# Kernel tuning notes

Hardware: AMD Instinct MI355X
Metric: run time of the kernel (lower is better)

Reference implementation:

```python
import jax, jax.numpy as jnp
import numpy as np

B, N, E = 128, 256, 2048
BINS = 16

def _gcn(x, src, dst, W, b):
    # GCNConv with self-loops and symmetric deg^-1/2 normalization (PyG default).
    h = x @ W  # [N, Fout]
    deg = jnp.zeros(x.shape[0], x.dtype).at[dst].add(1.0) + 1.0  # +1 self-loop
    dinv = jax.lax.rsqrt(deg)
    coef = dinv[src] * dinv[dst]  # [E]
    agg = jnp.zeros_like(h).at[dst].add(h[src] * coef[:, None])
    return agg + h / deg[:, None] + b  # self-loop norm = 1/deg

def _gnn(x, ei, W1, b1, W2, b2, W3, b3):
    # x: [B,N,Fin], ei: [B,2,E]. Dropout skipped (eval mode).
    def single(x, ei):
        s, d = ei[0], ei[1]
        h = jax.nn.relu(_gcn(x, s, d, W1, b1))
        h = jax.nn.relu(_gcn(h, s, d, W2, b2))
        return _gcn(h, s, d, W3, b3)
    return jax.vmap(single)(x, ei)

def _att_pool(x, Watt):
    # SimGNN attention pooling; all graphs have exactly N nodes.
    ctx = jnp.tanh((x @ Watt.T).sum(axis=1) / jnp.asarray(N, x.dtype))  # [B,f3]
    scores = jax.nn.sigmoid(jnp.einsum('bnf,bf->bn', x, ctx))  # [B,N]
    return jnp.einsum('bnf,bn->bf', x, scores)  # [B,f3]

def _forward(xq, xc, eq, ec, W1, b1, W2, b2, W3, b3, Watt, ntnW, ntnV, ntnb, fc1W, fc1b, fc2W, fc2b):
    q = _gnn(xq, eq, W1, b1, W2, b2, W3, b3)  # [B,N,f3]
    c = _gnn(xc, ec, W1, b1, W2, b2, W3, b3)
    e1 = _att_pool(q, Watt)
    e2 = _att_pool(c, Watt)
    # NTN: bilinear + linear on concat + bias
    scores = jax.nn.relu(
        jnp.einsum('bi,tij,bj->bt', e1, ntnW, e2)
        + jnp.concatenate([e1, e2], axis=-1) @ ntnV.T
        + ntnb
    )  # [B, tensor_neurons]
    # histogram of all pairwise node-embedding dot products (torch.histc semantics)
    s = jnp.einsum('bnf,bmf->bnm', q, c).ravel()
    lo, hi = s.min(), s.max()
    idx = jnp.clip(jnp.floor((s - lo) / (hi - lo) * BINS).astype(jnp.int32), 0, BINS - 1)
    counts = jnp.zeros(BINS, s.dtype).at[idx].add(1.0)
    h = jax.lax.stop_gradient(counts / counts.sum())
    scores = jnp.concatenate([scores, jnp.broadcast_to(h, (scores.shape[0], BINS))], axis=1)
    scores = jax.nn.relu(scores @ fc1W.T + fc1b)
    p = jax.nn.sigmoid(scores @ fc2W.T + fc2b)  # [B,1]
    return p.squeeze()


def setup_inputs() -> dict:
    key = jax.random.key(0)
    ks = jax.random.split(key, 20)
    Fin, f1, f2, f3, T, BN = 128, 128, 64, 32, 16, 16
    def xav(k, shape):
        fan_in, fan_out = shape[-1], shape[0]
        lim = np.sqrt(6.0 / (fan_in + fan_out))
        return jax.random.uniform(k, shape, jnp.float32, -lim, lim)
    return {
        'xq': jax.random.normal(ks[0], (B, N, Fin), jnp.float32),
        'xc': jax.random.normal(ks[1], (B, N, Fin), jnp.float32),
        'eq': jax.random.randint(ks[2], (B, 2, E), 0, N, jnp.int32),
        'ec': jax.random.randint(ks[3], (B, 2, E), 0, N, jnp.int32),
        'W1': xav(ks[4], (Fin, f1)), 'b1': jnp.zeros((f1,), jnp.float32),
        'W2': xav(ks[5], (f1, f2)), 'b2': jnp.zeros((f2,), jnp.float32),
        'W3': xav(ks[6], (f2, f3)), 'b3': jnp.zeros((f3,), jnp.float32),
        'Watt': xav(ks[7], (f3, f3)),
        'ntnW': xav(ks[8], (T, f3, f3)),
        'ntnV': xav(ks[9], (T, 2 * f3)),
        'ntnb': xav(ks[10], (T, 1)).squeeze(-1),
        'fc1W': xav(ks[11], (BN, T + BINS)), 'fc1b': jnp.zeros((BN,), jnp.float32),
        'fc2W': xav(ks[12], (1, BN)), 'fc2b': jnp.zeros((1,), jnp.float32),
    }


def reference(xq, xc, eq, ec, W1, b1, W2, b2, W3, b3, Watt, ntnW, ntnV, ntnb, fc1W, fc1b, fc2W, fc2b):
    return _forward(xq, xc, eq, ec, W1, b1, W2, b2, W3, b3, Watt, ntnW, ntnV, ntnb, fc1W, fc1b, fc2W, fc2b)
```

## Files before the change

### kernel.cpp

```cpp
#include <hip/hip_runtime.h>
#include <math.h>

#define BB 128
#define NN 256
#define EE 2048
#define BINS 16
#define HTS 36

__global__ void csr_kernel(const int* __restrict__ eq, const int* __restrict__ ec,
                           int* __restrict__ off, int* __restrict__ srcs,
                           float* __restrict__ wts) {
    int g = blockIdx.x;
    int b = g < BB ? g : g - BB;
    const int* ei = g < BB ? eq : ec;
    int t = threadIdx.x;
    __shared__ int cnt[NN];
    __shared__ int sa[NN], sb[NN];
    __shared__ int cursor[NN];
    __shared__ float dvs[NN];
    cnt[t] = 0;
    __syncthreads();
    const int* src = ei + b * 2 * EE;
    const int* dst = src + EE;
    for (int e = t; e < EE; e += 256) atomicAdd(&cnt[dst[e]], 1);
    __syncthreads();
    dvs[t] = rsqrtf((float)cnt[t] + 1.0f);
    sa[t] = cnt[t];
    __syncthreads();
    int* pin = sa; int* pout = sb;
    for (int d = 1; d < NN; d <<= 1) {
        int v = pin[t];
        if (t >= d) v += pin[t - d];
        pout[t] = v;
        __syncthreads();
        int* tmp = pin; pin = pout; pout = tmp;
    }
    int excl = pin[t] - cnt[t];
    off[g * 257 + t] = excl;
    if (t == 255) off[g * 257 + 256] = EE;
    cursor[t] = excl;
    __syncthreads();
    for (int e = t; e < EE; e += 256) {
        int d = dst[e], s = src[e];
        int pos = atomicAdd(&cursor[d], 1);
        srcs[g * EE + pos] = s;
        wts[g * EE + pos] = dvs[s] * dvs[d];
    }
}

template<int FIN, int FOUT, bool RELU>
__global__ __launch_bounds__(256, 2) void gcn_fused2(
        const float* __restrict__ X0, const float* __restrict__ X1,
        const float* __restrict__ W, const float* __restrict__ bias,
        const int* __restrict__ off, const int* __restrict__ srcs,
        const float* __restrict__ wts, float* __restrict__ OUT) {
    int blk = blockIdx.x;
    int g = blk % (2 * BB);
    int cb = (blk / (2 * BB)) * 32;
    int t = threadIdx.x;

    __shared__ float hT[NN * HTS];
    __shared__ float xsT[16 * 260];
    __shared__ float wt[16 * 32];
    __shared__ int   eoff[NN + 1];
    __shared__ int   esrc[EE];
    __shared__ float ewt[EE];

    const float* xg = (g < BB) ? (X0 + (size_t)g * NN * FIN)
                               : (X1 + (size_t)(g - BB) * NN * FIN);
    const int* o = off + g * 257;
    const int* sr = srcs + (size_t)g * EE;
    const float* wg = wts + (size_t)g * EE;

    for (int i = t; i < EE; i += 256) { esrc[i] = sr[i]; ewt[i] = wg[i]; }
    for (int i = t; i <= NN; i += 256) eoff[i] = o[i];

    int l = t & 63;
    int wv = t >> 6;

    float acc[4][8];
#pragma unroll
    for (int i = 0; i < 4; i++)
#pragma unroll
        for (int j = 0; j < 8; j++) acc[i][j] = 0.f;

    const float* xr = xg + t * FIN;
    float xa[16];
    *(float4*)&xa[0]  = *(const float4*)(xr);
    *(float4*)&xa[4]  = *(const float4*)(xr + 4);
    *(float4*)&xa[8]  = *(const float4*)(xr + 8);
    *(float4*)&xa[12] = *(const float4*)(xr + 12);
    int wrow = t >> 4, wcol = (t & 15) * 2;
    float2 wreg = *(const float2*)&W[wrow * FOUT + cb + wcol];

    for (int k0 = 0; k0 < FIN; k0 += 16) {
#pragma unroll
        for (int m = 0; m < 16; m++) xsT[m * 260 + t] = xa[m];
        *(float2*)&wt[wrow * 32 + wcol] = wreg;
        __syncthreads();
        if (k0 + 16 < FIN) {
            xr += 16;
            *(float4*)&xa[0]  = *(const float4*)(xr);
            *(float4*)&xa[4]  = *(const float4*)(xr + 4);
            *(float4*)&xa[8]  = *(const float4*)(xr + 8);
            *(float4*)&xa[12] = *(const float4*)(xr + 12);
            wreg = *(const float2*)&W[(k0 + 16 + wrow) * FOUT + cb + wcol];
        }
#pragma unroll
        for (int k = 0; k < 16; k++) {
            float4 xv = *(const float4*)&xsT[k * 260 + 4 * l];
            float4 wa = *(const float4*)&wt[k * 32 + 8 * wv];
            float4 wb = *(const float4*)&wt[k * 32 + 8 * wv + 4];
            float xq4[4] = {xv.x, xv.y, xv.z, xv.w};
            float wc8[8] = {wa.x, wa.y, wa.z, wa.w, wb.x, wb.y, wb.z, wb.w};
#pragma unroll
            for (int i = 0; i < 4; i++)
#pragma unroll
                for (int j = 0; j < 8; j++) acc[i][j] += xq4[i] * wc8[j];
        }
        __syncthreads();
    }
#pragma unroll
    for (int i = 0; i < 4; i++) {
        *(float4*)&hT[(4 * l + i) * HTS + 8 * wv] =
            make_float4(acc[i][0], acc[i][1], acc[i][2], acc[i][3]);
        *(float4*)&hT[(4 * l + i) * HTS + 8 * wv + 4] =
            make_float4(acc[i][4], acc[i][5], acc[i][6], acc[i][7]);
    }
    __syncthreads();

    int c = t & 31, ng = t >> 5;
    float bb_ = bias[cb + c];
    float* outp = OUT + (size_t)g * NN * FOUT;
    for (int n = ng; n < NN; n += 8) {
        int j0 = eoff[n], j1 = eoff[n + 1];
        float a = 0.f;
        int j = j0;
        if (j < j1) {
            int s0 = esrc[j];
            float w0 = ewt[j];
            for (++j; j < j1; ++j) {
                int s1 = esrc[j];
                float w1 = ewt[j];
                a += hT[s0 * HTS + c] * w0;
                s0 = s1; w0 = w1;
            }
            a += hT[s0 * HTS + c] * w0;
        }
        float d0i = 1.0f / ((float)(j1 - j0) + 1.0f);
        float val = a + hT[n * HTS + c] * d0i + bb_;
        if (RELU) val = fmaxf(val, 0.f);
        outp[n * FOUT + cb + c] = val;
    }
}

__global__ void attpool_kernel(const float* __restrict__ X, const float* __restrict__ Watt,
                               float* __restrict__ e) {
    int g = blockIdx.x;
    int t = threadIdx.x;
    __shared__ float xs[NN * 33];
    __shared__ float red[256];
    __shared__ float mean_s[32], ctx_s[32], sc[NN];
    const float* x = X + (size_t)g * NN * 32;
    for (int i = t; i < NN * 32; i += 256) { int n = i >> 5, c = i & 31; xs[n * 33 + c] = x[i]; }
    __syncthreads();
    {
        int c = t & 31, p = t >> 5;
        float s = 0.f;
        for (int n = p * 32; n < (p + 1) * 32; n++) s += xs[n * 33 + c];
        red[t] = s;
    }
    __syncthreads();
    if (t < 32) {
        float m = 0.f;
        for (int p = 0; p < 8; p++) m += red[p * 32 + t];
        mean_s[t] = m / (float)NN;
    }
    __syncthreads();
    if (t < 32) {
        float a = 0.f;
        for (int f = 0; f < 32; f++) a += mean_s[f] * Watt[t * 32 + f];
        ctx_s[t] = tanhf(a);
    }
    __syncthreads();
    {
        float a = 0.f;
        for (int f = 0; f < 32; f++) a += xs[t * 33 + f] * ctx_s[f];
        sc[t] = 1.f / (1.f + expf(-a));
    }
    __syncthreads();
    {
        int c = t & 31, p = t >> 5;
        float s = 0.f;
        for (int n = p * 32; n < (p + 1) * 32; n++) s += xs[n * 33 + c] * sc[n];
        red[t] = s;
    }
    __syncthreads();
    if (t < 32) {
        float s = 0.f;
        for (int p = 0; p < 8; p++) s += red[p * 32 + t];
        e[g * 32 + t] = s;
    }
}

#define PD_STAGE_AND_DOT \
    int blk = blockIdx.x; \
    int b = blk >> 2; \
    int tq = (blk >> 1) & 1, tc = blk & 1; \
    __shared__ float qsT[32 * 132]; \
    __shared__ float csT[32 * 132]; \
    int t = threadIdx.x; \
    { \
        int n = t >> 1, f0 = (t & 1) * 16; \
        const float* qp = Q + ((size_t)b * NN + tq * 128 + n) * 32 + f0; \
        const float* cp = C + ((size_t)b * NN + tc * 128 + n) * 32 + f0; \
        float qa16[16], ca16[16]; \
        *(float4*)&qa16[0]  = *(const float4*)(qp); \
        *(float4*)&qa16[4]  = *(const float4*)(qp + 4); \
        *(float4*)&qa16[8]  = *(const float4*)(qp + 8); \
        *(float4*)&qa16[12] = *(const float4*)(qp + 12); \
        *(float4*)&ca16[0]  = *(const float4*)(cp); \
        *(float4*)&ca16[4]  = *(const float4*)(cp + 4); \
        *(float4*)&ca16[8]  = *(const float4*)(cp + 8); \
        *(float4*)&ca16[12] = *(const float4*)(cp + 12); \
        _Pragma("unroll") \
        for (int m = 0; m < 16; m++) { \
            qsT[(f0 + m) * 132 + n] = qa16[m]; \
            csT[(f0 + m) * 132 + n] = ca16[m]; \
        } \
    } \
    __syncthreads(); \
    int rg = (t >> 4) * 4, cg = (t & 15) * 4; \
    float acc[8][8]; \
    _Pragma("unroll") \
    for (int i = 0; i < 8; i++) \
        _Pragma("unroll") \
        for (int j = 0; j < 8; j++) acc[i][j] = 0.f; \
    _Pragma("unroll 2") \
    for (int f = 0; f < 32; f++) { \
        float4 qa = *(const float4*)&qsT[f * 132 + rg]; \
        float4 qb = *(const float4*)&qsT[f * 132 + 64 + rg]; \
        float4 ca = *(const float4*)&csT[f * 132 + cg]; \
        float4 cb = *(const float4*)&csT[f * 132 + 64 + cg]; \
        float qv[8] = {qa.x, qa.y, qa.z, qa.w, qb.x, qb.y, qb.z, qb.w}; \
        float cv[8] = {ca.x, ca.y, ca.z, ca.w, cb.x, cb.y, cb.z, cb.w}; \
        _Pragma("unroll") \
        for (int i = 0; i < 8; i++) \
            _Pragma("unroll") \
            for (int j = 0; j < 8; j++) acc[i][j] += qv[i] * cv[j]; \
    }

__global__ __launch_bounds__(256, 4) void pairdot_minmax(
        const float* __restrict__ Q, const float* __restrict__ C,
        float* __restrict__ bmin, float* __restrict__ bmax) {
    PD_STAGE_AND_DOT
    float lmin = acc[0][0], lmax = acc[0][0];
#pragma unroll
    for (int i = 0; i < 8; i++)
#pragma unroll
        for (int j = 0; j < 8; j++) {
            lmin = fminf(lmin, acc[i][j]);
            lmax = fmaxf(lmax, acc[i][j]);
        }
    __shared__ float rmin[256], rmax[256];
    rmin[t] = lmin; rmax[t] = lmax;
    __syncthreads();
    for (int s = 128; s > 0; s >>= 1) {
        if (t < s) { rmin[t] = fminf(rmin[t], rmin[t + s]); rmax[t] = fmaxf(rmax[t], rmax[t + s]); }
        __syncthreads();
    }
    if (t == 0) { bmin[blk] = rmin[0]; bmax[blk] = rmax[0]; }
}

__global__ void minmax_kernel(const float* __restrict__ bmin, const float* __restrict__ bmax,
                              float* __restrict__ lohi, float* __restrict__ counts) {
    __shared__ float rmin[256], rmax[256];
    int t = threadIdx.x;
    float lmin = 1e30f, lmax = -1e30f;
    for (int i = t; i < 512; i += 256) { lmin = fminf(lmin, bmin[i]); lmax = fmaxf(lmax, bmax[i]); }
    rmin[t] = lmin; rmax[t] = lmax;
    __syncthreads();
    for (int s = 128; s > 0; s >>= 1) {
        if (t < s) { rmin[t] = fminf(rmin[t], rmin[t + s]); rmax[t] = fmaxf(rmax[t], rmax[t + s]); }
        __syncthreads();
    }
    if (t == 0) { lohi[0] = rmin[0]; lohi[1] = rmax[0]; }
    if (t < BINS) counts[t] = 0.f;
}

__global__ __launch_bounds__(256, 4) void pairdot_hist(
        const float* __restrict__ Q, const float* __restrict__ C,
        const float* __restrict__ lohi, float* __restrict__ counts) {
    PD_STAGE_AND_DOT
    float lo = lohi[0], hi = lohi[1];
    float scale = (float)BINS / (hi - lo);
    int lane = t & 63;
    int cnt = 0;
#pragma unroll
    for (int i = 0; i < 8; i++)
#pragma unroll
        for (int j = 0; j < 8; j++) {
            int idx = (int)floorf((acc[i][j] - lo) * scale);
            idx = min(max(idx, 0), BINS - 1);
            unsigned long long b0 = __ballot((idx & 1) != 0);
            unsigned long long b1 = __ballot((idx & 2) != 0);
            unsigned long long b2 = __ballot((idx & 4) != 0);
            unsigned long long b3 = __ballot((idx & 8) != 0);
            unsigned long long msk = ((lane & 1) ? b0 : ~b0);
            msk &= ((lane & 2) ? b1 : ~b1);
            msk &= ((lane & 4) ? b2 : ~b2);
            msk &= ((lane & 8) ? b3 : ~b3);
            cnt += __popcll(msk);
        }
    __shared__ float wbins[4][BINS];
    int wave = t >> 6;
    if (lane < BINS) wbins[wave][lane] = (float)cnt;
    __syncthreads();
    if (t < BINS) {
        atomicAdd(&counts[t], wbins[0][t] + wbins[1][t] + wbins[2][t] + wbins[3][t]);
    }
}

__global__ void final_kernel(const float* __restrict__ e1, const float* __restrict__ e2,
                             const float* __restrict__ ntnW, const float* __restrict__ ntnV,
                             const float* __restrict__ ntnb, const float* __restrict__ counts,
                             const float* __restrict__ fc1W, const float* __restrict__ fc1b,
                             const float* __restrict__ fc2W, const float* __restrict__ fc2b,
                             float* __restrict__ out) {
    int b = blockIdx.x;
    int t = threadIdx.x;
    __shared__ float a1[32], a2[32], red[256], z[32], u[16];
    if (t < 32) a1[t] = e1[b * 32 + t];
    else if (t < 64) a2[t - 32] = e2[b * 32 + t - 32];
    __syncthreads();
    int tt = t >> 4, g = t & 15;
    float p = 0.f;
#pragma unroll
    for (int ii = 0; ii < 2; ii++) {
        int i = g + 16 * ii;
        float d = 0.f;
        const float* wr = ntnW + (tt * 32 + i) * 32;
        for (int j = 0; j < 32; j++) d += wr[j] * a2[j];
        p += a1[i] * d;
    }
    red[t] = p;
    __syncthreads();
    if (t < 16) {
        float s = 0.f;
        for (int g2 = 0; g2 < 16; g2++) s += red[t * 16 + g2];
        float lin = ntnb[t];
        for (int i = 0; i < 32; i++) lin += ntnV[t * 64 + i] * a1[i];
        for (int i = 0; i < 32; i++) lin += ntnV[t * 64 + 32 + i] * a2[i];
        z[t] = fmaxf(s + lin, 0.f);
    } else if (t < 32) {
        float tot = 0.f;
        for (int i = 0; i < BINS; i++) tot += counts[i];
        z[t] = counts[t - 16] / tot;
    }
    __syncthreads();
    if (t < 16) {
        float a = fc1b[t];
        for (int i = 0; i < 32; i++) a += fc1W[t * 32 + i] * z[i];
        u[t] = fmaxf(a, 0.f);
    }
    __syncthreads();
    if (t == 0) {
        float a = fc2b[0];
        for (int i = 0; i < 16; i++) a += fc2W[i] * u[i];
        out[b] = 1.f / (1.f + expf(-a));
    }
}

extern "C" void kernel_launch(void* const* d_in, const int* in_sizes, int n_in,
                              void* d_out, int out_size, void* d_ws, size_t ws_size,
                              hipStream_t stream) {
    const float* xq   = (const float*)d_in[0];
    const float* xc   = (const float*)d_in[1];
    const int*   eq   = (const int*)d_in[2];
    const int*   ec   = (const int*)d_in[3];
    const float* W1   = (const float*)d_in[4];
    const float* b1   = (const float*)d_in[5];
    const float* W2   = (const float*)d_in[6];
    const float* b2   = (const float*)d_in[7];
    const float* W3   = (const float*)d_in[8];
    const float* b3   = (const float*)d_in[9];
    const float* Watt = (const float*)d_in[10];
    const float* ntnW = (const float*)d_in[11];
    const float* ntnV = (const float*)d_in[12];
    const float* ntnb = (const float*)d_in[13];
    const float* fc1W = (const float*)d_in[14];
    const float* fc1b = (const float*)d_in[15];
    const float* fc2W = (const float*)d_in[16];
    const float* fc2b = (const float*)d_in[17];
    float* out = (float*)d_out;
    float* ws  = (float*)d_ws;

    float* O3   = ws;
    float* e12  = O3 + 2097152;
    float* bmin = e12 + 8192;
    float* bmax = bmin + 2048;
    float* lohi = bmax + 2048;
    float* cntw = lohi + 2;
    int*   off  = (int*)(ws + 2109504);
    int*   srcs = off + 65792;
    float* wts  = (float*)(srcs + 524288);
    float* O1   = ws + 3223872;
    float* O2   = O1 + 8388608;

    float* O3Q = O3;
    float* O3C = O3 + (size_t)BB * NN * 32;
    float* e1w = e12;
    float* e2w = e12 + BB * 32;

    csr_kernel<<<2 * BB, 256, 0, stream>>>(eq, ec, off, srcs, wts);

    gcn_fused2<128, 128, true><<<4 * 2 * BB, 256, 0, stream>>>(
        xq, xc, W1, b1, off, srcs, wts, O1);
    gcn_fused2<128, 64, true><<<2 * 2 * BB, 256, 0, stream>>>(
        O1, O1 + (size_t)BB * NN * 128, W2, b2, off, srcs, wts, O2);
    gcn_fused2<64, 32, false><<<1 * 2 * BB, 256, 0, stream>>>(
        O2, O2 + (size_t)BB * NN * 64, W3, b3, off, srcs, wts, O3);

    attpool_kernel<<<2 * BB, 256, 0, stream>>>(O3, Watt, e12);

    pairdot_minmax<<<BB * 4, 256, 0, stream>>>(O3Q, O3C, bmin, bmax);
    minmax_kernel<<<1, 256, 0, stream>>>(bmin, bmax, lohi, cntw);
    pairdot_hist<<<BB * 4, 256, 0, stream>>>(O3Q, O3C, lohi, cntw);

    final_kernel<<<BB, 256, 0, stream>>>(e1w, e2w, ntnW, ntnV, ntnb, cntw,
                                         fc1W, fc1b, fc2W, fc2b, out);
}
```

Before: 309.9 us.

## Shrink GCN shared memory with u16 edge sources and on-the-fly edge weights

CSR edge sources are now stored as 16-bit indices, and per-edge weights are no longer materialized. Each GCN block loads per-node deg^-1/2 values into shared memory and forms the edge weights on the fly. The K-tile drops from 16 to 8 and launch bounds are raised to 3 blocks per CU to cut shared memory and registers and raise occupancy. The last layer splits its aggregation over node halves to double its block count. The trade-off is that every block recomputes the full GEMM for its half, and the gather loop does an extra shared-memory load and multiply per edge.

Result: slower. 327.9 us (+5.8%).

```diff
diff --git a/kernel.cpp b/kernel.cpp
--- a/kernel.cpp
+++ b/kernel.cpp
@@ -7,9 +7,11 @@
 #define BINS 16
 #define HTS 36
 
+typedef unsigned short u16;
+
 __global__ void csr_kernel(const int* __restrict__ eq, const int* __restrict__ ec,
-                           int* __restrict__ off, int* __restrict__ srcs,
-                           float* __restrict__ wts) {
+                           int* __restrict__ off, u16* __restrict__ srcs,
+                           float* __restrict__ dvsg) {
     int g = blockIdx.x;
     int b = g < BB ? g : g - BB;
     const int* ei = g < BB ? eq : ec;
@@ -17,14 +19,13 @@
     __shared__ int cnt[NN];
     __shared__ int sa[NN], sb[NN];
     __shared__ int cursor[NN];
-    __shared__ float dvs[NN];
     cnt[t] = 0;
     __syncthreads();
     const int* src = ei + b * 2 * EE;
     const int* dst = src + EE;
     for (int e = t; e < EE; e += 256) atomicAdd(&cnt[dst[e]], 1);
     __syncthreads();
-    dvs[t] = rsqrtf((float)cnt[t] + 1.0f);
+    dvsg[g * NN + t] = rsqrtf((float)cnt[t] + 1.0f);
     sa[t] = cnt[t];
     __syncthreads();
     int* pin = sa; int* pout = sb;
@@ -43,37 +44,39 @@
     for (int e = t; e < EE; e += 256) {
         int d = dst[e], s = src[e];
         int pos = atomicAdd(&cursor[d], 1);
-        srcs[g * EE + pos] = s;
-        wts[g * EE + pos] = dvs[s] * dvs[d];
-    }
-}
-
-template<int FIN, int FOUT, bool RELU>
-__global__ __launch_bounds__(256, 2) void gcn_fused2(
+        srcs[g * EE + pos] = (u16)s;
+    }
+}
+
+template<int FIN, int FOUT, bool RELU, int NSPLIT>
+__global__ __launch_bounds__(256, 3) void gcn_fused3(
         const float* __restrict__ X0, const float* __restrict__ X1,
         const float* __restrict__ W, const float* __restrict__ bias,
-        const int* __restrict__ off, const int* __restrict__ srcs,
-        const float* __restrict__ wts, float* __restrict__ OUT) {
+        const int* __restrict__ off, const u16* __restrict__ srcs,
+        const float* __restrict__ dvsg, float* __restrict__ OUT) {
+    constexpr int CHUNKS = FOUT / 32;
     int blk = blockIdx.x;
     int g = blk % (2 * BB);
-    int cb = (blk / (2 * BB)) * 32;
+    int rest = blk / (2 * BB);
+    int cb = (rest % CHUNKS) * 32;
+    int half = rest / CHUNKS;
     int t = threadIdx.x;
 
     __shared__ float hT[NN * HTS];
-    __shared__ float xsT[16 * 260];
-    __shared__ float wt[16 * 32];
+    __shared__ float xsT[8 * 260];
+    __shared__ float wt[8 * 32];
     __shared__ int   eoff[NN + 1];
-    __shared__ int   esrc[EE];
-    __shared__ float ewt[EE];
+    __shared__ u16   esrc[EE];
+    __shared__ float dvs_s[NN];
 
     const float* xg = (g < BB) ? (X0 + (size_t)g * NN * FIN)
                                : (X1 + (size_t)(g - BB) * NN * FIN);
     const int* o = off + g * 257;
-    const int* sr = srcs + (size_t)g * EE;
-    const float* wg = wts + (size_t)g * EE;
-
-    for (int i = t; i < EE; i += 256) { esrc[i] = sr[i]; ewt[i] = wg[i]; }
+    const u16* sr = srcs + (size_t)g * EE;
+
+    for (int i = t; i < EE; i += 256) esrc[i] = sr[i];
     for (int i = t; i <= NN; i += 256) eoff[i] = o[i];
+    dvs_s[t] = dvsg[g * NN + t];
 
     int l = t & 63;
     int wv = t >> 6;
@@ -85,29 +88,29 @@
         for (int j = 0; j < 8; j++) acc[i][j] = 0.f;
 
     const float* xr = xg + t * FIN;
-    float xa[16];
-    *(float4*)&xa[0]  = *(const float4*)(xr);
-    *(float4*)&xa[4]  = *(const float4*)(xr + 4);
-    *(float4*)&xa[8]  = *(const float4*)(xr + 8);
-    *(float4*)&xa[12] = *(const float4*)(xr + 12);
-    int wrow = t >> 4, wcol = (t & 15) * 2;
-    float2 wreg = *(const float2*)&W[wrow * FOUT + cb + wcol];
-
-    for (int k0 = 0; k0 < FIN; k0 += 16) {
-#pragma unroll
-        for (int m = 0; m < 16; m++) xsT[m * 260 + t] = xa[m];
-        *(float2*)&wt[wrow * 32 + wcol] = wreg;
+    float4 va = *(const float4*)(xr);
+    float4 vb = *(const float4*)(xr + 4);
+    int wrow = t >> 5, wcol = t & 31;
+    float wreg = W[wrow * FOUT + cb + wcol];
+
+    for (int k0 = 0; k0 < FIN; k0 += 8) {
+        xsT[0 * 260 + t] = va.x;
+        xsT[1 * 260 + t] = va.y;
+        xsT[2 * 260 + t] = va.z;
+        xsT[3 * 260 + t] = va.w;
+        xsT[4 * 260 + t] = vb.x;
+        xsT[5 * 260 + t] = vb.y;
+        xsT[6 * 260 + t] = vb.z;
+        xsT[7 * 260 + t] = vb.w;
+        wt[t] = wreg;
         __syncthreads();
-        if (k0 + 16 < FIN) {
-            xr += 16;
-            *(float4*)&xa[0]  = *(const float4*)(xr);
-            *(float4*)&xa[4]  = *(const float4*)(xr + 4);
-            *(float4*)&xa[8]  = *(const float4*)(xr + 8);
-            *(float4*)&xa[12] = *(const float4*)(xr + 12);
-            wreg = *(const float2*)&W[(k0 + 16 + wrow) * FOUT + cb + wcol];
-        }
-#pragma unroll
-        for (int k = 0; k < 16; k++) {
+        if (k0 + 8 < FIN) {
+            va = *(const float4*)(xr + k0 + 8);
+            vb = *(const float4*)(xr + k0 + 12);
+            wreg = W[(k0 + 8 + wrow) * FOUT + cb + wcol];
+        }
+#pragma unroll
+        for (int k = 0; k < 8; k++) {
             float4 xv = *(const float4*)&xsT[k * 260 + 4 * l];
             float4 wa = *(const float4*)&wt[k * 32 + 8 * wv];
             float4 wb = *(const float4*)&wt[k * 32 + 8 * wv + 4];
@@ -132,20 +135,22 @@
     int c = t & 31, ng = t >> 5;
     float bb_ = bias[cb + c];
     float* outp = OUT + (size_t)g * NN * FOUT;
-    for (int n = ng; n < NN; n += 8) {
+    constexpr int NSEG = NN / NSPLIT;
+    int nlo = half * NSEG, nhi = nlo + NSEG;
+    for (int n = nlo + ng; n < nhi; n += 8) {
         int j0 = eoff[n], j1 = eoff[n + 1];
+        float dn = dvs_s[n];
         float a = 0.f;
         int j = j0;
+        for (; j + 1 < j1; j += 2) {
+            int s0 = esrc[j], s1 = esrc[j + 1];
+            float w0 = dvs_s[s0] * dn, w1 = dvs_s[s1] * dn;
+            a += hT[s0 * HTS + c] * w0;
+            a += hT[s1 * HTS + c] * w1;
+        }
         if (j < j1) {
             int s0 = esrc[j];
-            float w0 = ewt[j];
-            for (++j; j < j1; ++j) {
-                int s1 = esrc[j];
-                float w1 = ewt[j];
-                a += hT[s0 * HTS + c] * w0;
-                s0 = s1; w0 = w1;
-            }
-            a += hT[s0 * HTS + c] * w0;
+            a += hT[s0 * HTS + c] * (dvs_s[s0] * dn);
         }
         float d0i = 1.0f / ((float)(j1 - j0) + 1.0f);
         float val = a + hT[n * HTS + c] * d0i + bb_;
@@ -402,8 +407,8 @@
     float* lohi = bmax + 2048;
     float* cntw = lohi + 2;
     int*   off  = (int*)(ws + 2109504);
-    int*   srcs = off + 65792;
-    float* wts  = (float*)(srcs + 524288);
+    u16*   srcs = (u16*)(off + 65792);
+    float* dvsg = ws + 2109504 + 65792 + 524288;
     float* O1   = ws + 3223872;
     float* O2   = O1 + 8388608;
 
@@ -412,14 +417,14 @@
     float* e1w = e12;
     float* e2w = e12 + BB * 32;
 
-    csr_kernel<<<2 * BB, 256, 0, stream>>>(eq, ec, off, srcs, wts);
-
-    gcn_fused2<128, 128, true><<<4 * 2 * BB, 256, 0, stream>>>(
-        xq, xc, W1, b1, off, srcs, wts, O1);
-    gcn_fused2<128, 64, true><<<2 * 2 * BB, 256, 0, stream>>>(
-        O1, O1 + (size_t)BB * NN * 128, W2, b2, off, srcs, wts, O2);
-    gcn_fused2<64, 32, false><<<1 * 2 * BB, 256, 0, stream>>>(
-        O2, O2 + (size_t)BB * NN * 64, W3, b3, off, srcs, wts, O3);
+    csr_kernel<<<2 * BB, 256, 0, stream>>>(eq, ec, off, srcs, dvsg);
+
+    gcn_fused3<128, 128, true, 1><<<4 * 2 * BB, 256, 0, stream>>>(
+        xq, xc, W1, b1, off, srcs, dvsg, O1);
+    gcn_fused3<128, 64, true, 1><<<2 * 2 * BB, 256, 0, stream>>>(
+        O1, O1 + (size_t)BB * NN * 128, W2, b2, off, srcs, dvsg, O2);
+    gcn_fused3<64, 32, false, 2><<<2 * 2 * BB, 256, 0, stream>>>(
+        O2, O2 + (size_t)BB * NN * 64, W3, b3, off, srcs, dvsg, O3);
 
     attpool_kernel<<<2 * BB, 256, 0, stream>>>(O3, Watt, e12);
 
```
